# Performance work log

Hardware: AMD Instinct MI355X
Metric: run time of the kernel (lower is better)

The kernel has to match this reference:

```python
import jax, jax.numpy as jnp
import numpy as np

TAU = 1.0
PAD_IDX = 0
EOS_IDX = 3
NEG = -10000000.0

B, T, H, E, V, BN = 256, 256, 1024, 512, 32000, 512


def setup_inputs() -> dict:
    key = jax.random.key(0)
    ks = jax.random.split(key, 30)
    s = lambda *sh: 0.02
    inp = {}
    inp['input_ids'] = jax.random.randint(ks[0], (B,), 0, V)
    inp['prediction'] = jax.random.normal(ks[1], (B, V), jnp.float32)
    inp['context'] = jax.random.normal(ks[2], (B, T, 2 * H), jnp.float32)
    inp['h0'] = jax.random.normal(ks[3], (2, B, H), jnp.float32)
    inp['mask'] = jax.random.randint(ks[4], (B, 8), 0, V)
    # parameters
    inp['embedding'] = jax.random.normal(ks[5], (V, E), jnp.float32) * 0.02
    inp['ge1_w'] = jax.random.normal(ks[6], (E, E), jnp.float32) * 0.02
    inp['ge1_b'] = jnp.zeros((E,), jnp.float32)
    inp['ge2_w'] = jax.random.normal(ks[7], (E, E), jnp.float32) * 0.02
    inp['ge2_b'] = jnp.zeros((E,), jnp.float32)
    inp['att_we'] = jax.random.normal(ks[8], (2 * H, H), jnp.float32) * 0.02
    inp['att_wd'] = jax.random.normal(ks[9], (H, H), jnp.float32) * 0.02
    inp['att_v'] = jax.random.normal(ks[10], (H,), jnp.float32) * 0.02
    in0 = 2 * H + E
    inp['wih0'] = jax.random.normal(ks[11], (3 * H, in0), jnp.float32) * 0.02
    inp['whh0'] = jax.random.normal(ks[12], (3 * H, H), jnp.float32) * 0.02
    inp['bih0'] = jnp.zeros((3 * H,), jnp.float32)
    inp['bhh0'] = jnp.zeros((3 * H,), jnp.float32)
    inp['wih1'] = jax.random.normal(ks[13], (3 * H, H), jnp.float32) * 0.02
    inp['whh1'] = jax.random.normal(ks[14], (3 * H, H), jnp.float32) * 0.02
    inp['bih1'] = jnp.zeros((3 * H,), jnp.float32)
    inp['bhh1'] = jnp.zeros((3 * H,), jnp.float32)
    inp['bn0_w'] = jax.random.normal(ks[15], (3 * H + E, BN), jnp.float32) * 0.02
    inp['bn0_b'] = jnp.zeros((BN,), jnp.float32)
    inp['bn1_w'] = jax.random.normal(ks[16], (BN, V), jnp.float32) * 0.02
    inp['bn1_b'] = jnp.zeros((V,), jnp.float32)
    return inp


def _gru_cell(x, h, wih, whh, bih, bhh):
    gi = x @ wih.T + bih  # [B, 3H]
    gh = h @ whh.T + bhh
    gi_r, gi_z, gi_n = jnp.split(gi, 3, axis=1)
    gh_r, gh_z, gh_n = jnp.split(gh, 3, axis=1)
    r = jax.nn.sigmoid(gi_r + gh_r)
    z = jax.nn.sigmoid(gi_z + gh_z)
    n = jnp.tanh(gi_n + r * gh_n)
    return (1.0 - z) * n + z * h


def _forward(input_ids, prediction, context, h0, mask, embedding,
             ge1_w, ge1_b, ge2_w, ge2_b, att_we, att_wd, att_v,
             wih0, whh0, bih0, bhh0, wih1, whh1, bih1, bhh1,
             bn0_w, bn0_b, bn1_w, bn1_b):
    embs = embedding[input_ids]  # [B, E]
    # global embedding gate
    probs = jax.nn.softmax(prediction / TAU, axis=1)  # [B, V]
    emb_avg = probs @ embedding  # [B, E]
    Hg = jax.nn.sigmoid(embs @ ge1_w + ge1_b + emb_avg @ ge2_w + ge2_b)
    embs = Hg * embs + (1.0 - Hg) * emb_avg
    # bahdanau attention with query = top-layer hidden
    q = h0[-1]  # [B, H]
    scores = jnp.tanh(context @ att_we + (q @ att_wd)[:, None, :]) @ att_v  # [B, T]
    attn = jax.nn.softmax(scores, axis=1)
    c_t = jnp.einsum('bt,btd->bd', attn, context)  # [B, 2H]
    rnn_in = jnp.concatenate([embs, c_t], axis=1)  # [B, E+2H]
    h1_0 = _gru_cell(rnn_in, h0[0], wih0, whh0, bih0, bhh0)
    h1_1 = _gru_cell(h1_0, h0[1], wih1, whh1, bih1, bhh1)
    output = h1_1
    h1 = jnp.stack([h1_0, h1_1])
    b0 = jnp.tanh(jnp.concatenate([output, c_t, embs], axis=1) @ bn0_w + bn0_b)
    pred = b0 @ bn1_w + bn1_b  # [B, V]
    # masked scatter: forbid already-generated tokens, but keep PAD/EOS columns
    pad_col = pred[:, PAD_IDX]
    eos_col = pred[:, EOS_IDX]
    rows = jnp.arange(pred.shape[0])
    pred = pred.at[rows[:, None], mask].set(NEG)
    pred = pred.at[:, PAD_IDX].set(pad_col)
    pred = pred.at[:, EOS_IDX].set(eos_col)
    return pred, h1, attn


def reference(input_ids, prediction, context, h0, mask, embedding,
              ge1_w, ge1_b, ge2_w, ge2_b, att_we, att_wd, att_v,
              wih0, whh0, bih0, bhh0, wih1, whh1, bih1, bhh1,
              bn0_w, bn0_b, bn1_w, bn1_b):
    return _forward(input_ids, prediction, context, h0, mask, embedding,
                    ge1_w, ge1_b, ge2_w, ge2_b, att_we, att_wd, att_v,
                    wih0, whh0, bih0, bhh0, wih1, whh1, bih1, bhh1,
                    bn0_w, bn0_b, bn1_w, bn1_b)
```

## Files before the change

### kernel.cpp

```cpp
#include <hip/hip_runtime.h>
#include <hip/hip_bf16.h>


typedef unsigned short u16;
typedef unsigned int u32;
typedef float f32x4 __attribute__((ext_vector_type(4)));
typedef u32 u32x4 __attribute__((ext_vector_type(4)));
typedef __bf16 bf16x8 __attribute__((ext_vector_type(8)));
typedef short s16x8 __attribute__((ext_vector_type(8)));

__device__ __forceinline__ u16 f2bf(float x) {
  u32 u = __float_as_uint(x);
  u += 0x7fffu + ((u >> 16) & 1u);
  return (u16)(u >> 16);
}
__device__ __forceinline__ u32 pack2(float a, float b) {
  return (u32)f2bf(a) | ((u32)f2bf(b) << 16);
}
__device__ __forceinline__ u32 cvt2(float a, float b) {
  union { __bf16 h[2]; u32 w; } u;
  u.h[0] = (__bf16)a; u.h[1] = (__bf16)b;
  return u.w;
}
__device__ __forceinline__ float bf2f(u16 v) {
  return __uint_as_float((u32)v << 16);
}
__device__ __forceinline__ f32x4 mfma_bf16(s16x8 a, s16x8 b, f32x4 c) {
  union { s16x8 s; bf16x8 b; } ua, ub;
  ua.s = a; ub.s = b;
  return __builtin_amdgcn_mfma_f32_16x16x32_bf16(ua.b, ub.b, c, 0, 0, 0);
}
__device__ __forceinline__ void gll16(const void* g, void* l) {
  __builtin_amdgcn_global_load_lds((__attribute__((address_space(1))) void*)g,
                                   (__attribute__((address_space(3))) void*)l,
                                   16, 0, 0);
}
__device__ __forceinline__ float sigf(float x) { return 1.0f / (1.0f + __expf(-x)); }

__global__ __launch_bounds__(512, 4) void k_scores_f32(
    const float* __restrict__ ctx, const u16* __restrict__ weT,
    const float* __restrict__ qd, const float* __restrict__ att_v,
    float* __restrict__ scores)
{
  __shared__ u16 As[2][4096];
  __shared__ u16 Bs[2][8192];

  const int tid = threadIdx.x;
  const int lane = tid & 63, wid = tid >> 6;
  const int l15 = lane & 15, lg = lane >> 4;
  const int wm = wid >> 2, wn = wid & 3;

  const int f = blockIdx.x;
  const int xcd = f & 7, slot = f >> 3;
  const int ntile = slot & 3;
  const int mtile = (slot >> 2) * 8 + xcd;
  const int n0 = ntile * 256;
  const int m0 = mtile * 128;
  const int b = mtile >> 1;

  const int arow = tid >> 2;
  const float* actx = ctx + (size_t)(m0 + arow) * 2048 + (tid & 3) * 8;
  const int awoff = arow * 32 + (((tid & 3) ^ ((arow >> 1) & 3)) * 8);

  const int sslot = ((lane & 3) ^ ((lane >> 3) & 3)) * 8;
  size_t bsrc[2];
#pragma unroll
  for (int i = 0; i < 2; ++i)
    bsrc[i] = (size_t)(n0 + (wid * 2 + i) * 16 + (lane >> 2)) * 2048 + sslot;

  const int rslot = (lg ^ ((l15 >> 1) & 3)) * 8;
  int aoff[4], boff[4];
#pragma unroll
  for (int mf = 0; mf < 4; ++mf) aoff[mf] = (wm * 64 + mf * 16 + l15) * 32 + rslot;
#pragma unroll
  for (int nf = 0; nf < 4; ++nf) boff[nf] = (wn * 64 + nf * 16 + l15) * 32 + rslot;

  f32x4 acc[4][4];
#pragma unroll
  for (int mf = 0; mf < 4; ++mf)
#pragma unroll
    for (int nf = 0; nf < 4; ++nf) acc[mf][nf] = (f32x4){0.f, 0.f, 0.f, 0.f};

  {
#pragma unroll
    for (int i = 0; i < 2; ++i)
      gll16(weT + bsrc[i], &Bs[0][(wid * 2 + i) * 512]);
    float4 a0 = *(const float4*)(actx);
    float4 a1 = *(const float4*)(actx + 4);
    u32x4 w = {cvt2(a0.x, a0.y), cvt2(a0.z, a0.w), cvt2(a1.x, a1.y), cvt2(a1.z, a1.w)};
    *(u32x4*)&As[0][awoff] = w;
  }
  __syncthreads();

  for (int kt = 0; kt < 64; ++kt) {
    const int cur = kt & 1, nxt = cur ^ 1;
    const bool pf = (kt < 63);
    float4 a0, a1;
    if (pf) {
#pragma unroll
      for (int i = 0; i < 2; ++i)
        gll16(weT + bsrc[i] + (size_t)(kt + 1) * 32, &Bs[nxt][(wid * 2 + i) * 512]);
      a0 = *(const float4*)(actx + (size_t)(kt + 1) * 32);
      a1 = *(const float4*)(actx + (size_t)(kt + 1) * 32 + 4);
    }
    s16x8 af[4], bf[4];
#pragma unroll
    for (int mf = 0; mf < 4; ++mf) af[mf] = *(const s16x8*)(&As[cur][0] + aoff[mf]);
#pragma unroll
    for (int nf = 0; nf < 4; ++nf) bf[nf] = *(const s16x8*)(&Bs[cur][0] + boff[nf]);
    __builtin_amdgcn_s_setprio(1);
#pragma unroll
    for (int nf = 0; nf < 4; ++nf)
#pragma unroll
      for (int mf = 0; mf < 4; ++mf)
        acc[mf][nf] = mfma_bf16(af[mf], bf[nf], acc[mf][nf]);
    __builtin_amdgcn_s_setprio(0);
    if (pf) {
      u32x4 w = {cvt2(a0.x, a0.y), cvt2(a0.z, a0.w), cvt2(a1.x, a1.y), cvt2(a1.z, a1.w)};
      *(u32x4*)&As[nxt][awoff] = w;
    }
    __syncthreads();
  }

  float rp[4][4] = {{0.f, 0.f, 0.f, 0.f}, {0.f, 0.f, 0.f, 0.f},
                    {0.f, 0.f, 0.f, 0.f}, {0.f, 0.f, 0.f, 0.f}};
#pragma unroll
  for (int nf = 0; nf < 4; ++nf) {
    int col = n0 + wn * 64 + nf * 16 + l15;
    float qv = qd[(size_t)b * 1024 + col];
    float vv = att_v[col];
#pragma unroll
    for (int mf = 0; mf < 4; ++mf)
#pragma unroll
      for (int e = 0; e < 4; ++e)
        rp[mf][e] += tanhf(acc[mf][nf][e] + qv) * vv;
  }
#pragma unroll
  for (int d = 1; d < 16; d <<= 1)
#pragma unroll
    for (int mf = 0; mf < 4; ++mf)
#pragma unroll
      for (int e = 0; e < 4; ++e)
        rp[mf][e] += __shfl_xor(rp[mf][e], d);
  if (l15 == 0) {
#pragma unroll
    for (int mf = 0; mf < 4; ++mf)
#pragma unroll
      for (int e = 0; e < 4; ++e)
        atomicAdd(&scores[(size_t)m0 + wm * 64 + mf * 16 + lg * 4 + e], rp[mf][e]);
  }
}

template <int MODE>
__global__ __launch_bounds__(256, 2) void k_gemm(
    const u16* __restrict__ A, const float* __restrict__ W,
    float* __restrict__ C, const float* __restrict__ bias,
    int N, int K, int ksteps_per, int tot_ksteps, int atomic_mode)
{
  __shared__ u16 As[2][8192];
  __shared__ u16 Bs[2][2048];
  const int tid = threadIdx.x, lane = tid & 63, wid = tid >> 6;
  const int l15 = lane & 15, lg = lane >> 4;
  const int m0 = blockIdx.x * 256;
  const int n0 = blockIdx.y * 64;
  const int kc0 = blockIdx.z * ksteps_per;
  int kcn = tot_ksteps - kc0;
  if (kcn > ksteps_per) kcn = ksteps_per;

  size_t asrc[4];
#pragma unroll
  for (int j = 0; j < 4; ++j)
    asrc[j] = (size_t)(m0 + wid * 64 + j * 16 + (lane >> 2)) * K + (size_t)(lane & 3) * 8;
  int aoff[4], boff[4];
#pragma unroll
  for (int mf = 0; mf < 4; ++mf) aoff[mf] = (wid * 64 + mf * 16 + l15) * 32 + lg * 8;
#pragma unroll
  for (int nf = 0; nf < 4; ++nf) boff[nf] = (nf * 16 + l15) * 32 + lg * 8;

  const int b_row = tid >> 2, b_c8 = tid & 3;
  const int b_kk = tid >> 3, b_c4 = tid & 7;

  f32x4 acc[4][4];
#pragma unroll
  for (int mf = 0; mf < 4; ++mf)
#pragma unroll
    for (int nf = 0; nf < 4; ++nf) acc[mf][nf] = (f32x4){0.f, 0.f, 0.f, 0.f};

  {
#pragma unroll
    for (int j = 0; j < 4; ++j)
      gll16(A + asrc[j] + (size_t)kc0 * 32, &As[0][wid * 2048 + j * 512]);
    if (MODE == 0) {
      const float* p = W + (size_t)(n0 + b_row) * K + (size_t)kc0 * 32 + b_c8 * 8;
      float4 v0 = *(const float4*)p, v1 = *(const float4*)(p + 4);
      u32* w = (u32*)&Bs[0][b_row * 32 + b_c8 * 8];
      w[0] = pack2(v0.x, v0.y); w[1] = pack2(v0.z, v0.w);
      w[2] = pack2(v1.x, v1.y); w[3] = pack2(v1.z, v1.w);
    } else {
      const float* p = W + (size_t)(kc0 * 32 + b_kk) * N + n0 + b_c4 * 4;
      float4 v0 = *(const float4*)p;
      float4 v1 = *(const float4*)(p + 32);
      int r0 = b_c4 * 4, r1 = 32 + b_c4 * 4;
      Bs[0][(r0 + 0) * 32 + b_kk] = f2bf(v0.x);
      Bs[0][(r0 + 1) * 32 + b_kk] = f2bf(v0.y);
      Bs[0][(r0 + 2) * 32 + b_kk] = f2bf(v0.z);
      Bs[0][(r0 + 3) * 32 + b_kk] = f2bf(v0.w);
      Bs[0][(r1 + 0) * 32 + b_kk] = f2bf(v1.x);
      Bs[0][(r1 + 1) * 32 + b_kk] = f2bf(v1.y);
      Bs[0][(r1 + 2) * 32 + b_kk] = f2bf(v1.z);
      Bs[0][(r1 + 3) * 32 + b_kk] = f2bf(v1.w);
    }
  }
  __syncthreads();

  for (int s = 0; s < kcn; ++s) {
    const int cur = s & 1, nxt = cur ^ 1;
    const bool pf = (s + 1 < kcn);
    const int ktn = kc0 + s + 1;
    float4 v0, v1;
    if (pf) {
#pragma unroll
      for (int j = 0; j < 4; ++j)
        gll16(A + asrc[j] + (size_t)ktn * 32, &As[nxt][wid * 2048 + j * 512]);
      if (MODE == 0) {
        const float* p = W + (size_t)(n0 + b_row) * K + (size_t)ktn * 32 + b_c8 * 8;
        v0 = *(const float4*)p; v1 = *(const float4*)(p + 4);
      } else {
        const float* p = W + (size_t)(ktn * 32 + b_kk) * N + n0 + b_c4 * 4;
        v0 = *(const float4*)p;
        v1 = *(const float4*)(p + 32);
      }
    }
    s16x8 af[4], bf[4];
#pragma unroll
    for (int mf = 0; mf < 4; ++mf) af[mf] = *(const s16x8*)(&As[cur][0] + aoff[mf]);
#pragma unroll
    for (int nf = 0; nf < 4; ++nf) bf[nf] = *(const s16x8*)(&Bs[cur][0] + boff[nf]);
#pragma unroll
    for (int nf = 0; nf < 4; ++nf)
#pragma unroll
      for (int mf = 0; mf < 4; ++mf)
        acc[mf][nf] = mfma_bf16(af[mf], bf[nf], acc[mf][nf]);
    if (pf) {
      if (MODE == 0) {
        u32* w = (u32*)&Bs[nxt][b_row * 32 + b_c8 * 8];
        w[0] = pack2(v0.x, v0.y); w[1] = pack2(v0.z, v0.w);
        w[2] = pack2(v1.x, v1.y); w[3] = pack2(v1.z, v1.w);
      } else {
        int r0 = b_c4 * 4, r1 = 32 + b_c4 * 4;
        Bs[nxt][(r0 + 0) * 32 + b_kk] = f2bf(v0.x);
        Bs[nxt][(r0 + 1) * 32 + b_kk] = f2bf(v0.y);
        Bs[nxt][(r0 + 2) * 32 + b_kk] = f2bf(v0.z);
        Bs[nxt][(r0 + 3) * 32 + b_kk] = f2bf(v0.w);
        Bs[nxt][(r1 + 0) * 32 + b_kk] = f2bf(v1.x);
        Bs[nxt][(r1 + 1) * 32 + b_kk] = f2bf(v1.y);
        Bs[nxt][(r1 + 2) * 32 + b_kk] = f2bf(v1.z);
        Bs[nxt][(r1 + 3) * 32 + b_kk] = f2bf(v1.w);
      }
    }
    __syncthreads();
  }

  const size_t Ns = (size_t)N;
#pragma unroll
  for (int mf = 0; mf < 4; ++mf)
#pragma unroll
    for (int nf = 0; nf < 4; ++nf) {
      int col = n0 + nf * 16 + l15;
#pragma unroll
      for (int e = 0; e < 4; ++e) {
        int row = m0 + wid * 64 + mf * 16 + lg * 4 + e;
        float v = acc[mf][nf][e];
        if (atomic_mode) atomicAdd(&C[row * Ns + col], v);
        else C[row * Ns + col] = v + (bias ? bias[col] : 0.0f);
      }
    }
}

__global__ __launch_bounds__(256) void k_prep(
    const float* __restrict__ we, u16* __restrict__ weT,
    const float* __restrict__ h0, u16* __restrict__ h0_bf,
    const int* __restrict__ ids, const float* __restrict__ emb,
    float* __restrict__ e0, u16* __restrict__ e0b)
{
  __shared__ float t[32][33];
  const int bid = blockIdx.x, tid = threadIdx.x;
  if (bid < 2048) {
    const int n0 = (bid & 31) * 32, k0 = (bid >> 5) * 32;
#pragma unroll
    for (int p = 0; p < 4; ++p) {
      int e = tid + p * 256, r = e >> 5, c = e & 31;
      t[r][c] = we[(size_t)(k0 + r) * 1024 + n0 + c];
    }
    __syncthreads();
#pragma unroll
    for (int p = 0; p < 4; ++p) {
      int e = tid + p * 256, n = e >> 5, k = e & 31;
      weT[(size_t)(n0 + n) * 2048 + k0 + k] = f2bf(t[k][n]);
    }
  } else if (bid < 4096) {
    int i = (bid - 2048) * 256 + tid;
    h0_bf[i] = f2bf(h0[i]);
  } else {
    int b = bid - 4096;
    int id = ids[b];
    for (int i = tid; i < 512; i += 256) {
      float v = emb[(size_t)id * 512 + i];
      e0[(size_t)b * 512 + i] = v;
      e0b[(size_t)b * 512 + i] = f2bf(v);
    }
  }
}

__global__ void k_cast(const float* __restrict__ s, u16* __restrict__ d, int n)
{
  int i = blockIdx.x * 256 + threadIdx.x;
  if (i < n) d[i] = f2bf(s[i]);
}

__global__ __launch_bounds__(1024) void k_softmax_pred(const float* __restrict__ pred,
                                                       u16* __restrict__ probs)
{
  __shared__ u16 xrow[32000];
  __shared__ float smM[16], smS[16];
  const int row = blockIdx.x, tid = threadIdx.x;
  const float* x = pred + (size_t)row * 32000;
  float m = -3.0e38f, s = 0.f;
  for (int i = tid; i < 32000; i += 1024) {
    u16 bv = f2bf(x[i]);
    xrow[i] = bv;
    float vr = bf2f(bv);
    if (vr > m) { s = s * __expf(m - vr) + 1.0f; m = vr; }
    else s += __expf(vr - m);
  }
#pragma unroll
  for (int d = 1; d < 64; d <<= 1) {
    float mo = __shfl_xor(m, d), so = __shfl_xor(s, d);
    float M = fmaxf(m, mo);
    s = s * __expf(m - M) + so * __expf(mo - M);
    m = M;
  }
  if ((tid & 63) == 0) { smM[tid >> 6] = m; smS[tid >> 6] = s; }
  __syncthreads();
  float M = -3.0e38f;
#pragma unroll
  for (int w = 0; w < 16; ++w) M = fmaxf(M, smM[w]);
  float S = 0.f;
#pragma unroll
  for (int w = 0; w < 16; ++w) S += smS[w] * __expf(smM[w] - M);
  float inv = 1.0f / S;
  for (int i = tid; i < 32000; i += 1024)
    probs[(size_t)row * 32000 + i] = f2bf(__expf(bf2f(xrow[i]) - M) * inv);
}

__global__ __launch_bounds__(256) void k_attn_ct(
    const float* __restrict__ sc, const float* __restrict__ ctx,
    float* __restrict__ attn, float* __restrict__ c_t)
{
  __shared__ float sm[4];
  __shared__ float att[256];
  const int b = blockIdx.y, tid = threadIdx.x;
  float x = sc[(size_t)b * 256 + tid];
  float mx = x;
#pragma unroll
  for (int d = 1; d < 64; d <<= 1) mx = fmaxf(mx, __shfl_xor(mx, d));
  if ((tid & 63) == 0) sm[tid >> 6] = mx;
  __syncthreads();
  mx = fmaxf(fmaxf(sm[0], sm[1]), fmaxf(sm[2], sm[3]));
  float e = __expf(x - mx);
  float s = e;
#pragma unroll
  for (int d = 1; d < 64; d <<= 1) s += __shfl_xor(s, d);
  __syncthreads();
  if ((tid & 63) == 0) sm[tid >> 6] = s;
  __syncthreads();
  s = sm[0] + sm[1] + sm[2] + sm[3];
  float a = e / s;
  att[tid] = a;
  if (blockIdx.x == 0) attn[(size_t)b * 256 + tid] = a;
  __syncthreads();

  const int d0 = blockIdx.x * 512 + tid * 2;
  const float2* cp = (const float2*)(ctx + (size_t)b * 524288 + d0);
  float a0 = 0.f, a1 = 0.f;
#pragma unroll 8
  for (int t = 0; t < 256; ++t) {
    float av = att[t];
    float2 v = cp[(size_t)t * 1024];
    a0 += av * v.x; a1 += av * v.y;
  }
  float2* o = (float2*)(c_t + (size_t)b * 2048 + d0);
  *o = (float2){a0, a1};
}

__global__ void k_gate_cat(const float* __restrict__ gepre, const float* __restrict__ b1,
                           const float* __restrict__ b2, const float* __restrict__ e0,
                           const float* __restrict__ ea, float* __restrict__ embs,
                           const float* __restrict__ ct, u16* __restrict__ out)
{
  int i = blockIdx.x * 256 + threadIdx.x;
  int m = i / 2560, c = i - m * 2560;
  float v;
  if (c < 512) {
    int idx = m * 512 + c;
    float hg = sigf(gepre[idx] + b1[c] + b2[c]);
    v = hg * e0[idx] + (1.0f - hg) * ea[idx];
    embs[idx] = v;
  } else {
    v = ct[(size_t)m * 2048 + (c - 512)];
  }
  out[i] = f2bf(v);
}

__global__ void k_gru(const float* __restrict__ gi, const float* __restrict__ gh,
                      const float* __restrict__ bih, const float* __restrict__ bhh,
                      const float* __restrict__ hprev, float* __restrict__ hout,
                      u16* __restrict__ hout_bf)
{
  int i = blockIdx.x * 256 + threadIdx.x;
  int m = i >> 10, h = i & 1023;
  const float* gim = gi + (size_t)m * 3072;
  const float* ghm = gh + (size_t)m * 3072;
  float r = sigf(gim[h] + bih[h] + ghm[h] + bhh[h]);
  float z = sigf(gim[1024 + h] + bih[1024 + h] + ghm[1024 + h] + bhh[1024 + h]);
  float n = tanhf(gim[2048 + h] + bih[2048 + h] + r * (ghm[2048 + h] + bhh[2048 + h]));
  float hv = (1.0f - z) * n + z * hprev[i];
  hout[i] = hv;
  if (hout_bf) hout_bf[i] = f2bf(hv);
}

__global__ void k_cat_bn0(const float* __restrict__ h11, const float* __restrict__ ct,
                          const float* __restrict__ embs, u16* __restrict__ out)
{
  int i = blockIdx.x * 256 + threadIdx.x;
  int m = i / 3584, c = i - m * 3584;
  float v;
  if (c < 1024) v = h11[(size_t)m * 1024 + c];
  else if (c < 3072) v = ct[(size_t)m * 2048 + (c - 1024)];
  else v = embs[(size_t)m * 512 + (c - 3072)];
  out[i] = f2bf(v);
}

__global__ void k_bn0(const float* __restrict__ pre, const float* __restrict__ bias,
                      u16* __restrict__ b0b)
{
  int i = blockIdx.x * 256 + threadIdx.x;
  int nn = i & 511;
  b0b[i] = f2bf(tanhf(pre[i] + bias[nn]));
}

__global__ void k_mask(const int* __restrict__ mask, float* __restrict__ pred)
{
  int t = blockIdx.x * 256 + threadIdx.x;
  if (t >= 2048) return;
  int b = t >> 3;
  int col = mask[t];
  if (col != 0 && col != 3) pred[(size_t)b * 32000 + col] = -10000000.0f;
}

extern "C" void kernel_launch(void* const* d_in, const int* in_sizes, int n_in,
                              void* d_out, int out_size, void* d_ws, size_t ws_size,
                              hipStream_t stream)
{
  const int*   input_ids = (const int*)d_in[0];
  const float* prediction= (const float*)d_in[1];
  const float* context   = (const float*)d_in[2];
  const float* h0        = (const float*)d_in[3];
  const int*   maskp     = (const int*)d_in[4];
  const float* embedding = (const float*)d_in[5];
  const float* ge1_w = (const float*)d_in[6];
  const float* ge1_b = (const float*)d_in[7];
  const float* ge2_w = (const float*)d_in[8];
  const float* ge2_b = (const float*)d_in[9];
  const float* att_we = (const float*)d_in[10];
  const float* att_wd = (const float*)d_in[11];
  const float* att_v  = (const float*)d_in[12];
  const float* wih0 = (const float*)d_in[13];
  const float* whh0 = (const float*)d_in[14];
  const float* bih0 = (const float*)d_in[15];
  const float* bhh0 = (const float*)d_in[16];
  const float* wih1 = (const float*)d_in[17];
  const float* whh1 = (const float*)d_in[18];
  const float* bih1 = (const float*)d_in[19];
  const float* bhh1 = (const float*)d_in[20];
  const float* bn0_w = (const float*)d_in[21];
  const float* bn0_b = (const float*)d_in[22];
  const float* bn1_w = (const float*)d_in[23];
  const float* bn1_b = (const float*)d_in[24];

  float* out = (float*)d_out;
  float* out_pred = out;
  float* out_h1_0 = out + 8192000;
  float* out_h1_1 = out + 8454144;
  float* out_attn = out + 8716288;

  char* ws = (char*)d_ws;
  float* qd      = (float*)(ws + 0);
  float* emb_avg = (float*)(ws + 1048576);
  float* gepre   = (float*)(ws + 1572864);
  float* gi0     = (float*)(ws + 2097152);
  float* gh0     = (float*)(ws + 5242880);
  float* gi1     = (float*)(ws + 8388608);
  float* gh1     = (float*)(ws + 11534336);
  float* bn0pre  = (float*)(ws + 14680064);
  float* scores  = (float*)(ws + 15204352);
  const size_t MS_BYTES = 15466496;
  float* c_t     = (float*)(ws + 15466496);
  float* embs0   = (float*)(ws + 17563648);
  float* embs    = (float*)(ws + 18087936);
  u16* weT       = (u16*)(ws + 18612224);
  u16* h0_bf     = (u16*)(ws + 22806528);
  u16* embs0_bf  = (u16*)(ws + 23855104);
  u16* probs_bf  = (u16*)(ws + 24117248);
  u16* embavg_bf = (u16*)(ws + 40501248);
  u16* rnnin_bf  = (u16*)(ws + 40763392);
  u16* h1_0_bf   = (u16*)(ws + 42074112);
  u16* bn0in_bf  = (u16*)(ws + 42598400);
  u16* b0_bf     = (u16*)(ws + 44433408);

  (void)in_sizes; (void)n_in; (void)out_size; (void)ws_size;

  hipMemsetAsync(ws, 0, MS_BYTES, stream);

  k_prep<<<4352, 256, 0, stream>>>(att_we, weT, h0, h0_bf, input_ids, embedding,
                                   embs0, embs0_bf);
  k_softmax_pred<<<256, 1024, 0, stream>>>(prediction, probs_bf);

  k_gemm<1><<<dim3(1, 16, 8), 256, 0, stream>>>(h0_bf + 262144, att_wd, qd, nullptr,
                                                1024, 1024, 4, 32, 1);
  k_scores_f32<<<2048, 512, 0, stream>>>(context, weT, qd, att_v, scores);

  k_gemm<1><<<dim3(1, 8, 50), 256, 0, stream>>>(probs_bf, embedding, emb_avg, nullptr,
                                                512, 32000, 20, 1000, 1);
  k_cast<<<512, 256, 0, stream>>>(emb_avg, embavg_bf, 131072);
  k_gemm<1><<<dim3(1, 8, 4), 256, 0, stream>>>(embs0_bf, ge1_w, gepre, nullptr,
                                               512, 512, 4, 16, 1);
  k_gemm<1><<<dim3(1, 8, 4), 256, 0, stream>>>(embavg_bf, ge2_w, gepre, nullptr,
                                               512, 512, 4, 16, 1);

  k_attn_ct<<<dim3(4, 256), 256, 0, stream>>>(scores, context, out_attn, c_t);

  k_gate_cat<<<2560, 256, 0, stream>>>(gepre, ge1_b, ge2_b, embs0, emb_avg,
                                       embs, c_t, rnnin_bf);

  k_gemm<0><<<dim3(1, 48, 5), 256, 0, stream>>>(rnnin_bf, wih0, gi0, nullptr,
                                                3072, 2560, 16, 80, 1);
  k_gemm<0><<<dim3(1, 48, 4), 256, 0, stream>>>(h0_bf, whh0, gh0, nullptr,
                                                3072, 1024, 8, 32, 1);
  k_gru<<<1024, 256, 0, stream>>>(gi0, gh0, bih0, bhh0, h0, out_h1_0, h1_0_bf);
  k_gemm<0><<<dim3(1, 48, 4), 256, 0, stream>>>(h1_0_bf, wih1, gi1, nullptr,
                                                3072, 1024, 8, 32, 1);
  k_gemm<0><<<dim3(1, 48, 4), 256, 0, stream>>>(h0_bf + 262144, whh1, gh1, nullptr,
                                                3072, 1024, 8, 32, 1);
  k_gru<<<1024, 256, 0, stream>>>(gi1, gh1, bih1, bhh1, h0 + 262144, out_h1_1, nullptr);

  k_cat_bn0<<<3584, 256, 0, stream>>>(out_h1_1, c_t, embs, bn0in_bf);
  k_gemm<1><<<dim3(1, 8, 16), 256, 0, stream>>>(bn0in_bf, bn0_w, bn0pre, nullptr,
                                                512, 3584, 7, 112, 1);
  k_bn0<<<512, 256, 0, stream>>>(bn0pre, bn0_b, b0_bf);
  k_gemm<1><<<dim3(1, 500, 1), 256, 0, stream>>>(b0_bf, bn1_w, out_pred, bn1_b,
                                                 32000, 512, 16, 16, 0);
  k_mask<<<8, 256, 0, stream>>>(maskp, out_pred);
}
```

Before: 781.3 us.

## Emit bf16 context copy from scores kernel and use it for context vector

The scores kernel already converts the fp32 context to bf16 for its MFMA tiles. It now also writes that bf16 copy to workspace, but only from the n-tile 0 blocks. A new attention/context-vector kernel reads this half-size copy instead of the fp32 context, cutting the HBM traffic of the second pass over the 512MB context. This adds a 256MB write, lowers the precision of c_t to bf16 inputs, and runs only when the workspace is large enough.

```diff
diff --git a/kernel.cpp b/kernel.cpp
--- a/kernel.cpp
+++ b/kernel.cpp
@@ -40,7 +40,7 @@
 __global__ __launch_bounds__(512, 4) void k_scores_f32(
     const float* __restrict__ ctx, const u16* __restrict__ weT,
     const float* __restrict__ qd, const float* __restrict__ att_v,
-    float* __restrict__ scores)
+    float* __restrict__ scores, u16* __restrict__ cbf)
 {
   __shared__ u16 As[2][4096];
   __shared__ u16 Bs[2][8192];
@@ -61,6 +61,8 @@
   const int arow = tid >> 2;
   const float* actx = ctx + (size_t)(m0 + arow) * 2048 + (tid & 3) * 8;
   const int awoff = arow * 32 + (((tid & 3) ^ ((arow >> 1) & 3)) * 8);
+  u16* cbw = (ntile == 0 && cbf) ?
+      (cbf + (size_t)(m0 + arow) * 2048 + (tid & 3) * 8) : nullptr;
 
   const int sslot = ((lane & 3) ^ ((lane >> 3) & 3)) * 8;
   size_t bsrc[2];
@@ -89,6 +91,7 @@
     float4 a1 = *(const float4*)(actx + 4);
     u32x4 w = {cvt2(a0.x, a0.y), cvt2(a0.z, a0.w), cvt2(a1.x, a1.y), cvt2(a1.z, a1.w)};
     *(u32x4*)&As[0][awoff] = w;
+    if (cbw) *(u32x4*)cbw = w;
   }
   __syncthreads();
 
@@ -118,6 +121,7 @@
     if (pf) {
       u32x4 w = {cvt2(a0.x, a0.y), cvt2(a0.z, a0.w), cvt2(a1.x, a1.y), cvt2(a1.z, a1.w)};
       *(u32x4*)&As[nxt][awoff] = w;
+      if (cbw) *(u32x4*)(cbw + (size_t)(kt + 1) * 32) = w;
     }
     __syncthreads();
   }
@@ -351,6 +355,46 @@
   float inv = 1.0f / S;
   for (int i = tid; i < 32000; i += 1024)
     probs[(size_t)row * 32000 + i] = f2bf(__expf(bf2f(xrow[i]) - M) * inv);
+}
+
+__global__ __launch_bounds__(256) void k_attn_ct_bf(
+    const float* __restrict__ sc, const u16* __restrict__ ctxb,
+    float* __restrict__ attn, float* __restrict__ c_t)
+{
+  __shared__ float sm[4];
+  __shared__ float att[256];
+  const int b = blockIdx.y, tid = threadIdx.x;
+  float x = sc[(size_t)b * 256 + tid];
+  float mx = x;
+#pragma unroll
+  for (int d = 1; d < 64; d <<= 1) mx = fmaxf(mx, __shfl_xor(mx, d));
+  if ((tid & 63) == 0) sm[tid >> 6] = mx;
+  __syncthreads();
+  mx = fmaxf(fmaxf(sm[0], sm[1]), fmaxf(sm[2], sm[3]));
+  float e = __expf(x - mx);
+  float s = e;
+#pragma unroll
+  for (int d = 1; d < 64; d <<= 1) s += __shfl_xor(s, d);
+  __syncthreads();
+  if ((tid & 63) == 0) sm[tid >> 6] = s;
+  __syncthreads();
+  s = sm[0] + sm[1] + sm[2] + sm[3];
+  float a = e / s;
+  att[tid] = a;
+  if (blockIdx.x == 0) attn[(size_t)b * 256 + tid] = a;
+  __syncthreads();
+
+  const int d0 = blockIdx.x * 512 + tid * 2;
+  const u16* cp = ctxb + (size_t)b * 524288 + d0;
+  float a0 = 0.f, a1 = 0.f;
+#pragma unroll 8
+  for (int t = 0; t < 256; ++t) {
+    float av = att[t];
+    ushort2 v = *(const ushort2*)(cp + (size_t)t * 2048);
+    a0 += av * bf2f(v.x); a1 += av * bf2f(v.y);
+  }
+  float2* o = (float2*)(c_t + (size_t)b * 2048 + d0);
+  *o = (float2){a0, a1};
 }
 
 __global__ __launch_bounds__(256) void k_attn_ct(
@@ -517,8 +561,10 @@
   u16* h1_0_bf   = (u16*)(ws + 42074112);
   u16* bn0in_bf  = (u16*)(ws + 42598400);
   u16* b0_bf     = (u16*)(ws + 44433408);
-
-  (void)in_sizes; (void)n_in; (void)out_size; (void)ws_size;
+  u16* ctx_bf    = (u16*)(ws + 44695552);
+  const bool big = ws_size >= 44695552ull + 268435456ull;
+
+  (void)in_sizes; (void)n_in; (void)out_size;
 
   hipMemsetAsync(ws, 0, MS_BYTES, stream);
 
@@ -528,7 +574,8 @@
 
   k_gemm<1><<<dim3(1, 16, 8), 256, 0, stream>>>(h0_bf + 262144, att_wd, qd, nullptr,
                                                 1024, 1024, 4, 32, 1);
-  k_scores_f32<<<2048, 512, 0, stream>>>(context, weT, qd, att_v, scores);
+  k_scores_f32<<<2048, 512, 0, stream>>>(context, weT, qd, att_v, scores,
+                                         big ? ctx_bf : nullptr);
 
   k_gemm<1><<<dim3(1, 8, 50), 256, 0, stream>>>(probs_bf, embedding, emb_avg, nullptr,
                                                 512, 32000, 20, 1000, 1);
@@ -538,7 +585,10 @@
   k_gemm<1><<<dim3(1, 8, 4), 256, 0, stream>>>(embavg_bf, ge2_w, gepre, nullptr,
                                                512, 512, 4, 16, 1);
 
-  k_attn_ct<<<dim3(4, 256), 256, 0, stream>>>(scores, context, out_attn, c_t);
+  if (big)
+    k_attn_ct_bf<<<dim3(4, 256), 256, 0, stream>>>(scores, ctx_bf, out_attn, c_t);
+  else
+    k_attn_ct<<<dim3(4, 256), 256, 0, stream>>>(scores, context, out_attn, c_t);
 
   k_gate_cat<<<2560, 256, 0, stream>>>(gepre, ge1_b, ge2_b, embs0, emb_avg,
                                        embs, c_t, rnnin_bf);
```

Result: no change. 786.5 us (+0.7%).
